# Performance work log

Hardware: AMD Instinct MI355X
Metric: run time of the kernel (lower is better)

The kernel has to match this reference:

```python
import jax, jax.numpy as jnp
import numpy as np

B, T, S, D, VOCAB = 16, 64, 128, 512, 32000


def setup_inputs():
    key = jax.random.key(0)
    ks = jax.random.split(key, 20)
    w = lambda i, shape: jax.random.normal(ks[i], shape, dtype=jnp.float32) * 0.05
    return {
        'words': jax.random.randint(ks[0], (B, T), 0, VOCAB),
        'encoder_output': jax.random.normal(ks[1], (B, S, D), dtype=jnp.float32),
        'pre_h': jax.random.normal(ks[2], (B, D), dtype=jnp.float32),
        'cell': jax.random.normal(ks[3], (B, D), dtype=jnp.float32),
        'emb': w(4, (VOCAB, D)),
        'W_ih': w(5, (4 * D, D)), 'W_hh': w(6, (4 * D, D)),
        'b_ih': w(7, (4 * D,)), 'b_hh': w(8, (4 * D,)),
        'Wh_w': w(9, (D, D)),
        'Ws_w': w(10, (D, D)), 'Ws_b': w(11, (D,)),
        'vt_w': w(12, (D,)),
        'V_w': w(13, (D, 2 * D)), 'V_b': w(14, (D,)),
        'Vp_w': w(15, (VOCAB, D)), 'Vp_b': w(16, (VOCAB,)),
    }


def lstm(xs, h0, c0, W_ih, W_hh, b_ih, b_hh):
    # xs: [T, B, D]; PyTorch LSTM gate order: i, f, g, o
    def step(carry, x_t):
        h, c = carry
        g = x_t @ W_ih.T + b_ih + h @ W_hh.T + b_hh
        i, f, gg, o = jnp.split(g, 4, axis=-1)
        c = jax.nn.sigmoid(f) * c + jax.nn.sigmoid(i) * jnp.tanh(gg)
        h = jax.nn.sigmoid(o) * jnp.tanh(c)
        return (h, c), h
    _, hs = jax.lax.scan(step, (h0, c0), xs)
    return hs


def reference(words, encoder_output, pre_h, cell, emb, W_ih, W_hh, b_ih, b_hh,
              Wh_w, Ws_w, Ws_b, vt_w, V_w, V_b, Vp_w, Vp_b):
    x = emb[words]                                   # [B, T, D]
    hs = lstm(x.transpose(1, 0, 2), pre_h, cell, W_ih, W_hh, b_ih, b_hh)
    out = hs.transpose(1, 0, 2)                      # [B, T, D] decoder states
    wh = encoder_output @ Wh_w.T                     # [B, S, D]
    ws = out @ Ws_w.T + Ws_b                         # [B, T, D]
    # Bahdanau additive attention scores e[b,s,t] = v_t . tanh(wh[b,s] + ws[b,t])
    e = jnp.einsum('bstd,d->bst', jnp.tanh(wh[:, :, None, :] + ws[:, None, :, :]), vt_w)
    a = jax.nn.softmax(e, axis=1)                    # softmax over source positions
    context = jnp.einsum('bst,bsd->btd', a, encoder_output)
    cat = jnp.concatenate([context, out], axis=-1)   # [B, T, 2D]
    return (cat @ V_w.T + V_b) @ Vp_w.T + Vp_b       # [B, T, VOCAB]
```

## Files before the change

### kernel.cpp

```cpp
#include <hip/hip_runtime.h>

#define DEV __device__ __forceinline__

typedef float f32x4 __attribute__((ext_vector_type(4)));
typedef short s16x8 __attribute__((ext_vector_type(8)));
typedef unsigned short u16;
typedef u16 u16x4 __attribute__((ext_vector_type(4)));
typedef u16 u16x8 __attribute__((ext_vector_type(8)));
typedef unsigned int u32x4 __attribute__((ext_vector_type(4)));

constexpr int Bb = 16, Tt = 64, Ss = 128, Dd = 512, Vv = 32000, FD = 2048;

DEV u16 f2bf(float x) {
  unsigned u = __builtin_bit_cast(unsigned, x);
  u = u + 0x7fffu + ((u >> 16) & 1u);
  return (u16)(u >> 16);
}
DEV float bf2f(u16 h) { unsigned u = ((unsigned)h) << 16; return __builtin_bit_cast(float, u); }
DEV float sigm(float x) { return 1.f / (1.f + __expf(-x)); }
DEV float ftanh(float x) {
  x = fminf(15.f, fmaxf(-15.f, x));
  float e = __expf(2.f * x);
  return (e - 1.f) / (e + 1.f);
}

__global__ void k_cvt3(const float* __restrict__ i0, u16* __restrict__ o0, int n0,
                       const float* __restrict__ i1, u16* __restrict__ o1, int n1,
                       const float* __restrict__ i2, u16* __restrict__ o2, int n2) {
  int total = n0 + n1 + n2;
  int i = blockIdx.x * blockDim.x + threadIdx.x;
  int st = gridDim.x * blockDim.x;
  for (; i < total; i += st) {
    const float* in; u16* out; int j;
    if (i < n0) { in = i0; out = o0; j = i; }
    else if (i < n0 + n1) { in = i1; out = o1; j = i - n0; }
    else { in = i2; out = o2; j = i - n0 - n1; }
    float4 v = reinterpret_cast<const float4*>(in)[j];
    u16x4 o;
    o.x = f2bf(v.x); o.y = f2bf(v.y); o.z = f2bf(v.z); o.w = f2bf(v.w);
    reinterpret_cast<u16x4*>(out)[j] = o;
  }
}

DEV void cvt_split_one(const float* __restrict__ in, u16* __restrict__ hi,
                       u16* __restrict__ lo, int i) {
  float4 v = reinterpret_cast<const float4*>(in)[i];
  u16x4 oh, ol;
  float vv[4] = {v.x, v.y, v.z, v.w};
#pragma unroll
  for (int j = 0; j < 4; ++j) {
    u16 h = f2bf(vv[j]);
    oh[j] = h;
    ol[j] = f2bf(vv[j] - bf2f(h));
  }
  reinterpret_cast<u16x4*>(hi)[i] = oh;
  reinterpret_cast<u16x4*>(lo)[i] = ol;
}

__global__ void k_cvt_split(const float* __restrict__ in, u16* __restrict__ hi,
                            u16* __restrict__ lo, int n4) {
  int i = blockIdx.x * blockDim.x + threadIdx.x;
  int st = gridDim.x * blockDim.x;
  for (; i < n4; i += st) cvt_split_one(in, hi, lo, i);
}

__global__ void k_cvt_split2(const float* __restrict__ a, u16* __restrict__ ah, u16* __restrict__ al,
                             const float* __restrict__ b, u16* __restrict__ bh, u16* __restrict__ bl,
                             int n4) {
  int i = blockIdx.x * blockDim.x + threadIdx.x;
  int st = gridDim.x * blockDim.x;
  if (blockIdx.y == 0) { for (; i < n4; i += st) cvt_split_one(a, ah, al, i); }
  else                 { for (; i < n4; i += st) cvt_split_one(b, bh, bl, i); }
}

__global__ void k_prep(const int* __restrict__ words, const float* __restrict__ emb,
                       u16* __restrict__ xb,
                       const float* __restrict__ pre, unsigned* __restrict__ hp0,
                       const float* __restrict__ bi, const float* __restrict__ bh,
                       float* __restrict__ bsum) {
  int blk = blockIdx.x, tid = threadIdx.x;
  if (blk < Bb * Tt) {
    int row = words[blk];
    int d = tid * 2;
    float2 v = *reinterpret_cast<const float2*>(&emb[(size_t)row * Dd + d]);
    xb[(size_t)blk * Dd + d] = f2bf(v.x);
    xb[(size_t)blk * Dd + d + 1] = f2bf(v.y);
  } else if (blk < Bb * Tt + 32) {
    int i = (blk - Bb * Tt) * 256 + tid;
    float v = pre[i];
    u16 h = f2bf(v);
    u16 l = f2bf(v - bf2f(h));
    hp0[i] = (unsigned)h | ((unsigned)l << 16);
  } else {
    int i = (blk - Bb * Tt - 32) * 256 + tid;
    bsum[i] = bi[i] + bh[i];
  }
}

template <bool BIAS, bool OUTBF, int TERMS>
__global__ __launch_bounds__(256) void k_gemm(const u16* __restrict__ A,
                                              const u16* __restrict__ Al,
                                              const u16* __restrict__ Bm,
                                              const u16* __restrict__ Bl,
                                              float* __restrict__ Cf, u16* __restrict__ Cb,
                                              const float* __restrict__ bias,
                                              int M, int N, int K) {
  constexpr int NTILE = (TERMS == 3) ? 4 : 2;
  __shared__ u16 ls[NTILE * 128 * 32];
  u16* lsA = ls;
  u16* lsB = ls + 128 * 32;
  u16* lsAl = ls + 2 * 128 * 32;
  u16* lsBl = ls + 3 * 128 * 32;
  const int mt = M >> 7;
  const int tm = (blockIdx.x % mt) << 7;
  const int tn = (blockIdx.x / mt) << 7;
  const int tid = threadIdx.x;
  const int wave = tid >> 6, lane = tid & 63;
  const int wr = wave >> 1, wc = wave & 1;
  f32x4 acc[4][4];
#pragma unroll
  for (int i = 0; i < 4; ++i)
#pragma unroll
    for (int j = 0; j < 4; ++j) acc[i][j] = (f32x4){0.f, 0.f, 0.f, 0.f};

  const int lrow = lane >> 2;
  const int lk = (lane & 3) << 3;
  const int fr = lane & 15, fk = (lane >> 4) << 3;

  for (int k0 = 0; k0 < K; k0 += 32) {
#pragma unroll
    for (int r = 0; r < 2; ++r) {
      int rowA = r * 64 + wave * 16;
      size_t goffA = (size_t)(tm + rowA + lrow) * K + k0 + lk;
      size_t goffB = (size_t)(tn + rowA + lrow) * K + k0 + lk;
      __builtin_amdgcn_global_load_lds((const __attribute__((address_space(1))) void*)(A + goffA),
                                       (__attribute__((address_space(3))) void*)&lsA[rowA * 32],
                                       16, 0, 0);
      __builtin_amdgcn_global_load_lds((const __attribute__((address_space(1))) void*)(Bm + goffB),
                                       (__attribute__((address_space(3))) void*)&lsB[rowA * 32],
                                       16, 0, 0);
      if constexpr (TERMS == 3) {
        __builtin_amdgcn_global_load_lds((const __attribute__((address_space(1))) void*)(Al + goffA),
                                         (__attribute__((address_space(3))) void*)&lsAl[rowA * 32],
                                         16, 0, 0);
        __builtin_amdgcn_global_load_lds((const __attribute__((address_space(1))) void*)(Bl + goffB),
                                         (__attribute__((address_space(3))) void*)&lsBl[rowA * 32],
                                         16, 0, 0);
      }
    }
    __syncthreads();
    s16x8 av[4], bv[4];
#pragma unroll
    for (int mi = 0; mi < 4; ++mi)
      av[mi] = *reinterpret_cast<const s16x8*>(&lsA[(wr * 64 + mi * 16 + fr) * 32 + fk]);
#pragma unroll
    for (int ni = 0; ni < 4; ++ni)
      bv[ni] = *reinterpret_cast<const s16x8*>(&lsB[(wc * 64 + ni * 16 + fr) * 32 + fk]);
    if constexpr (TERMS == 3) {
      s16x8 avl[4], bvl[4];
#pragma unroll
      for (int mi = 0; mi < 4; ++mi)
        avl[mi] = *reinterpret_cast<const s16x8*>(&lsAl[(wr * 64 + mi * 16 + fr) * 32 + fk]);
#pragma unroll
      for (int ni = 0; ni < 4; ++ni)
        bvl[ni] = *reinterpret_cast<const s16x8*>(&lsBl[(wc * 64 + ni * 16 + fr) * 32 + fk]);
#pragma unroll
      for (int mi = 0; mi < 4; ++mi)
#pragma unroll
        for (int ni = 0; ni < 4; ++ni) {
          acc[mi][ni] = __builtin_amdgcn_mfma_f32_16x16x32_bf16(av[mi], bv[ni], acc[mi][ni], 0, 0, 0);
          acc[mi][ni] = __builtin_amdgcn_mfma_f32_16x16x32_bf16(av[mi], bvl[ni], acc[mi][ni], 0, 0, 0);
          acc[mi][ni] = __builtin_amdgcn_mfma_f32_16x16x32_bf16(avl[mi], bv[ni], acc[mi][ni], 0, 0, 0);
        }
    } else {
#pragma unroll
      for (int mi = 0; mi < 4; ++mi)
#pragma unroll
        for (int ni = 0; ni < 4; ++ni)
          acc[mi][ni] = __builtin_amdgcn_mfma_f32_16x16x32_bf16(av[mi], bv[ni], acc[mi][ni], 0, 0, 0);
    }
    __syncthreads();
  }

  const int fm = (lane >> 4) << 2;
#pragma unroll
  for (int ni = 0; ni < 4; ++ni) {
    int col = tn + wc * 64 + ni * 16 + fr;
    float badd = 0.f;
    if constexpr (BIAS) badd = bias[col];
#pragma unroll
    for (int mi = 0; mi < 4; ++mi) {
#pragma unroll
      for (int r = 0; r < 4; ++r) {
        int row = tm + wr * 64 + mi * 16 + fm + r;
        size_t idx = (size_t)row * N + col;
        float v = acc[mi][ni][r] + badd;
        if constexpr (OUTBF) Cb[idx] = f2bf(v);
        else Cf[idx] = v;
      }
    }
  }
}

__global__ __launch_bounds__(256) void k_lstm(const float* __restrict__ xg,
                                              const float* __restrict__ Whh,
                                              const float* __restrict__ cell,
                                              unsigned* __restrict__ hpack,
                                              u16* __restrict__ out_hi,
                                              u16* __restrict__ out_lo,
                                              int* __restrict__ flags) {
  const int w = blockIdx.x;
  const int tid = threadIdx.x;
  const int gi = tid >> 6, lane = tid & 63;
  const int ds0 = w << 4;
  __shared__ float g_lds[4][16][16];

  const int fr = lane & 15;
  const int fkb = (lane >> 4) << 3;

  s16x8 whi[16], wlo[16];
  {
    const float* wrow = Whh + (size_t)(gi * Dd + ds0 + fr) * Dd;
#pragma unroll
    for (int kc = 0; kc < 16; ++kc) {
      int k = kc * 32 + fkb;
      float4 a = *reinterpret_cast<const float4*>(&wrow[k]);
      float4 b = *reinterpret_cast<const float4*>(&wrow[k + 4]);
      float vv[8] = {a.x, a.y, a.z, a.w, b.x, b.y, b.z, b.w};
#pragma unroll
      for (int j = 0; j < 8; ++j) {
        u16 h = f2bf(vv[j]);
        whi[kc][j] = (short)h;
        wlo[kc][j] = (short)f2bf(vv[j] - bf2f(h));
      }
    }
  }

  const int ub = tid >> 4, ud = tid & 15;
  float c = cell[(size_t)ub * Dd + ds0 + ud];

  for (int t = 0; t < Tt; ++t) {
    float xgv[4];
#pragma unroll
    for (int r = 0; r < 4; ++r) {
      int bb = ((lane >> 4) << 2) + r;
      xgv[r] = xg[(size_t)(bb * Tt + t) * FD + gi * Dd + ds0 + fr];
    }
#pragma unroll
    for (int r = 0; r < 4; ++r) asm volatile("" ::"v"(xgv[r]));

    if (t > 0) {
      if (gi == 0) {
        if (lane < 32 && lane != w) {
          while (__hip_atomic_load(&flags[lane * 32], __ATOMIC_RELAXED,
                                   __HIP_MEMORY_SCOPE_AGENT) < t) {}
          while (__hip_atomic_load(&flags[lane * 32], __ATOMIC_ACQUIRE,
                                   __HIP_MEMORY_SCOPE_AGENT) < t) {}
        }
        __builtin_amdgcn_sched_barrier(0);
      }
      __syncthreads();
    }

    const unsigned* hp = hpack + (size_t)t * (Bb * Dd) + (size_t)fr * Dd;
    f32x4 a0 = (f32x4){0.f, 0.f, 0.f, 0.f};
    f32x4 a1 = a0, a2 = a0;
#pragma unroll
    for (int kc = 0; kc < 16; ++kc) {
      int k = kc * 32 + fkb;
      u32x4 u0 = *reinterpret_cast<const u32x4*>(&hp[k]);
      u32x4 u1 = *reinterpret_cast<const u32x4*>(&hp[k + 4]);
      s16x8 ahi, alo;
#pragma unroll
      for (int j = 0; j < 4; ++j) {
        ahi[j] = (short)(u0[j] & 0xffffu); alo[j] = (short)(u0[j] >> 16);
        ahi[4 + j] = (short)(u1[j] & 0xffffu); alo[4 + j] = (short)(u1[j] >> 16);
      }
      a0 = __builtin_amdgcn_mfma_f32_16x16x32_bf16(ahi, whi[kc], a0, 0, 0, 0);
      a1 = __builtin_amdgcn_mfma_f32_16x16x32_bf16(ahi, wlo[kc], a1, 0, 0, 0);
      a2 = __builtin_amdgcn_mfma_f32_16x16x32_bf16(alo, whi[kc], a2, 0, 0, 0);
    }
#pragma unroll
    for (int r = 0; r < 4; ++r) {
      int bb = ((lane >> 4) << 2) + r;
      g_lds[gi][bb][fr] = a0[r] + a1[r] + a2[r] + xgv[r];
    }
    __syncthreads();
    float iv = g_lds[0][ub][ud], fv = g_lds[1][ub][ud];
    float gv = g_lds[2][ub][ud], ov = g_lds[3][ub][ud];
    c = sigm(fv) * c + sigm(iv) * ftanh(gv);
    float h = sigm(ov) * ftanh(c);
    u16 hh = f2bf(h);
    u16 hl = f2bf(h - bf2f(hh));
    unsigned pk = (unsigned)hh | ((unsigned)hl << 16);
    __hip_atomic_store(&hpack[(size_t)(t + 1) * (Bb * Dd) + ub * Dd + ds0 + ud], pk,
                       __ATOMIC_RELAXED, __HIP_MEMORY_SCOPE_AGENT);
    size_t oidx = (size_t)(ub * Tt + t) * Dd + ds0 + ud;
    out_hi[oidx] = hh;
    out_lo[oidx] = hl;
    __syncthreads();
    if (tid == 0)
      __hip_atomic_store(&flags[w * 32], t + 1, __ATOMIC_RELAXED, __HIP_MEMORY_SCOPE_AGENT);
  }
}

__global__ __launch_bounds__(256) void k_attn(const float* __restrict__ wh,
                                              const float* __restrict__ wst,
                                              const float* __restrict__ vt,
                                              const float* __restrict__ enc,
                                              const u16* __restrict__ out_hi,
                                              u16* __restrict__ cat) {
  const int tid = threadIdx.x;
  const int wave = tid >> 6, lane = tid & 63;
  const int wid = blockIdx.x * 4 + wave;
  const int b = wid >> 6, t = wid & 63;
  const int d0 = lane << 3;

  float wsv[8], vtv[8];
  {
    const float4* p = reinterpret_cast<const float4*>(&wst[(size_t)(b * Tt + t) * Dd + d0]);
    float4 x = p[0], y = p[1];
    wsv[0] = x.x; wsv[1] = x.y; wsv[2] = x.z; wsv[3] = x.w;
    wsv[4] = y.x; wsv[5] = y.y; wsv[6] = y.z; wsv[7] = y.w;
    const float4* q = reinterpret_cast<const float4*>(&vt[d0]);
    float4 u = q[0], v = q[1];
    vtv[0] = u.x; vtv[1] = u.y; vtv[2] = u.z; vtv[3] = u.w;
    vtv[4] = v.x; vtv[5] = v.y; vtv[6] = v.z; vtv[7] = v.w;
  }
  float e0 = 0.f, e1 = 0.f;
  for (int s = 0; s < Ss; ++s) {
    const float4* p = reinterpret_cast<const float4*>(&wh[(size_t)(b * Ss + s) * Dd + d0]);
    float4 x = p[0], y = p[1];
    float whv[8] = {x.x, x.y, x.z, x.w, y.x, y.y, y.z, y.w};
    float a = 0.f;
#pragma unroll
    for (int j = 0; j < 8; ++j) a += ftanh(whv[j] + wsv[j]) * vtv[j];
#pragma unroll
    for (int off = 32; off; off >>= 1) a += __shfl_xor(a, off);
    if (lane == (s & 63)) { if (s < 64) e0 = a; else e1 = a; }
  }
  float m = fmaxf(e0, e1);
#pragma unroll
  for (int off = 32; off; off >>= 1) m = fmaxf(m, __shfl_xor(m, off));
  float p0 = __expf(e0 - m), p1 = __expf(e1 - m);
  float sum = p0 + p1;
#pragma unroll
  for (int off = 32; off; off >>= 1) sum += __shfl_xor(sum, off);
  float inv = 1.f / sum;
  float a0 = p0 * inv, a1 = p1 * inv;

  float ctx[8] = {0.f, 0.f, 0.f, 0.f, 0.f, 0.f, 0.f, 0.f};
  for (int s = 0; s < Ss; ++s) {
    float as = __shfl(s < 64 ? a0 : a1, s & 63);
    const float4* p = reinterpret_cast<const float4*>(&enc[(size_t)(b * Ss + s) * Dd + d0]);
    float4 x = p[0], y = p[1];
    ctx[0] += as * x.x; ctx[1] += as * x.y; ctx[2] += as * x.z; ctx[3] += as * x.w;
    ctx[4] += as * y.x; ctx[5] += as * y.y; ctx[6] += as * y.z; ctx[7] += as * y.w;
  }
  u16x8 co;
#pragma unroll
  for (int j = 0; j < 8; ++j) co[j] = f2bf(ctx[j]);
  size_t cbase = (size_t)(b * Tt + t) * (2 * Dd);
  *reinterpret_cast<u16x8*>(&cat[cbase + d0]) = co;
  u16x8 ov = *reinterpret_cast<const u16x8*>(&out_hi[(size_t)(b * Tt + t) * Dd + d0]);
  *reinterpret_cast<u16x8*>(&cat[cbase + Dd + d0]) = ov;
}

extern "C" void kernel_launch(void* const* d_in, const int* in_sizes, int n_in,
                              void* d_out, int out_size, void* d_ws, size_t ws_size,
                              hipStream_t stream) {
  const int* words = (const int*)d_in[0];
  const float* enc = (const float*)d_in[1];
  const float* pre_h = (const float*)d_in[2];
  const float* cell = (const float*)d_in[3];
  const float* emb = (const float*)d_in[4];
  const float* W_ih = (const float*)d_in[5];
  const float* W_hh = (const float*)d_in[6];
  const float* b_ih = (const float*)d_in[7];
  const float* b_hh = (const float*)d_in[8];
  const float* Wh_w = (const float*)d_in[9];
  const float* Ws_w = (const float*)d_in[10];
  const float* Ws_b = (const float*)d_in[11];
  const float* vt_w = (const float*)d_in[12];
  const float* V_w = (const float*)d_in[13];
  const float* V_b = (const float*)d_in[14];
  const float* Vp_w = (const float*)d_in[15];
  const float* Vp_b = (const float*)d_in[16];
  float* outp = (float*)d_out;

  char* ws = (char*)d_ws;
  size_t off = 0;
  auto alloc = [&](size_t bytes) {
    char* p = ws + off;
    off = (off + bytes + 255) & ~(size_t)255;
    return p;
  };
  int* flags = (int*)alloc(4096);
  float* xg = (float*)alloc((size_t)Bb * Tt * FD * 4);
  float* wh = (float*)alloc((size_t)Bb * Ss * Dd * 4);
  float* wst = (float*)alloc((size_t)Bb * Tt * Dd * 4);
  unsigned* hpack = (unsigned*)alloc((size_t)(Tt + 1) * Bb * Dd * 4);
  u16* out_hi = (u16*)alloc((size_t)Bb * Tt * Dd * 2);
  u16* out_lo = (u16*)alloc((size_t)Bb * Tt * Dd * 2);
  u16* x_bf = (u16*)alloc((size_t)Bb * Tt * Dd * 2);
  u16* enc_hi = (u16*)alloc((size_t)Bb * Ss * Dd * 2);
  u16* enc_lo = (u16*)alloc((size_t)Bb * Ss * Dd * 2);
  u16* Wih_bf = (u16*)alloc((size_t)FD * Dd * 2);
  u16* Whw_hi = (u16*)alloc((size_t)Dd * Dd * 2);
  u16* Whw_lo = (u16*)alloc((size_t)Dd * Dd * 2);
  u16* Wsw_hi = (u16*)alloc((size_t)Dd * Dd * 2);
  u16* Wsw_lo = (u16*)alloc((size_t)Dd * Dd * 2);
  u16* Vw_bf = (u16*)alloc((size_t)Dd * 2 * Dd * 2);
  u16* Vp_bf = (u16*)alloc((size_t)Vv * Dd * 2);
  u16* cat = (u16*)alloc((size_t)Bb * Tt * 2 * Dd * 2);
  u16* hmid = (u16*)alloc((size_t)Bb * Tt * Dd * 2);
  float* bsum = (float*)alloc((size_t)FD * 4);
  if (off > ws_size) return;

  hipMemsetAsync(flags, 0, 4096, stream);

  k_cvt3<<<2048, 256, 0, stream>>>(W_ih, Wih_bf, FD * Dd / 4,
                                   V_w, Vw_bf, Dd * 2 * Dd / 4,
                                   Vp_w, Vp_bf, Vv * Dd / 4);
  k_cvt_split<<<1024, 256, 0, stream>>>(enc, enc_hi, enc_lo, Bb * Ss * Dd / 4);
  k_cvt_split2<<<dim3(256, 2), 256, 0, stream>>>(Wh_w, Whw_hi, Whw_lo,
                                                 Ws_w, Wsw_hi, Wsw_lo, Dd * Dd / 4);
  k_prep<<<Bb * Tt + 32 + 8, 256, 0, stream>>>(words, emb, x_bf, pre_h, (unsigned*)hpack,
                                               b_ih, b_hh, bsum);

  k_gemm<true, false, 1><<<8 * 16, 256, 0, stream>>>(x_bf, nullptr, Wih_bf, nullptr,
                                                     xg, nullptr, bsum, 1024, 2048, 512);
  k_gemm<false, false, 3><<<16 * 4, 256, 0, stream>>>(enc_hi, enc_lo, Whw_hi, Whw_lo,
                                                      wh, nullptr, nullptr, 2048, 512, 512);
  k_lstm<<<32, 256, 0, stream>>>(xg, W_hh, cell, (unsigned*)hpack, out_hi, out_lo, flags);
  k_gemm<true, false, 3><<<8 * 4, 256, 0, stream>>>(out_hi, out_lo, Wsw_hi, Wsw_lo,
                                                    wst, nullptr, Ws_b, 1024, 512, 512);
  k_attn<<<256, 256, 0, stream>>>(wh, wst, vt_w, enc, out_hi, cat);
  k_gemm<true, true, 1><<<8 * 4, 256, 0, stream>>>(cat, nullptr, Vw_bf, nullptr,
                                                   nullptr, hmid, V_b, 1024, 512, 1024);
  k_gemm<true, false, 1><<<8 * 250, 256, 0, stream>>>(hmid, nullptr, Vp_bf, nullptr,
                                                      outp, nullptr, Vp_b, 1024, 32000, 512);
}
```

Baseline: 629.9 us.

## Overlap LSTM recurrence with Wh GEMM and weight conversions in one launch

Merges the sequential LSTM kernel with the encoder Wh projection GEMM and the conversion of Vp, V and Ws weights into one 256-block launch, with blocks dispatched by index. The idle GPU capacity during the latency-bound 32-block recurrence is used for independent work that previously ran serially. The pre-LSTM conversions are also merged into a single kernel. This risks the LSTM blocks' spin-wait progress depending on co-resident blocks, and contention for memory bandwidth slowing the critical recurrence path.

```diff
diff --git a/kernel.cpp b/kernel.cpp
--- a/kernel.cpp
+++ b/kernel.cpp
@@ -24,22 +24,11 @@
   return (e - 1.f) / (e + 1.f);
 }
 
-__global__ void k_cvt3(const float* __restrict__ i0, u16* __restrict__ o0, int n0,
-                       const float* __restrict__ i1, u16* __restrict__ o1, int n1,
-                       const float* __restrict__ i2, u16* __restrict__ o2, int n2) {
-  int total = n0 + n1 + n2;
-  int i = blockIdx.x * blockDim.x + threadIdx.x;
-  int st = gridDim.x * blockDim.x;
-  for (; i < total; i += st) {
-    const float* in; u16* out; int j;
-    if (i < n0) { in = i0; out = o0; j = i; }
-    else if (i < n0 + n1) { in = i1; out = o1; j = i - n0; }
-    else { in = i2; out = o2; j = i - n0 - n1; }
-    float4 v = reinterpret_cast<const float4*>(in)[j];
-    u16x4 o;
-    o.x = f2bf(v.x); o.y = f2bf(v.y); o.z = f2bf(v.z); o.w = f2bf(v.w);
-    reinterpret_cast<u16x4*>(out)[j] = o;
-  }
+DEV void cvt_plain_one(const float* __restrict__ in, u16* __restrict__ out, int i) {
+  float4 v = reinterpret_cast<const float4*>(in)[i];
+  u16x4 o;
+  o.x = f2bf(v.x); o.y = f2bf(v.y); o.z = f2bf(v.z); o.w = f2bf(v.w);
+  reinterpret_cast<u16x4*>(out)[i] = o;
 }
 
 DEV void cvt_split_one(const float* __restrict__ in, u16* __restrict__ hi,
@@ -57,20 +46,19 @@
   reinterpret_cast<u16x4*>(lo)[i] = ol;
 }
 
-__global__ void k_cvt_split(const float* __restrict__ in, u16* __restrict__ hi,
-                            u16* __restrict__ lo, int n4) {
+__global__ void k_cvt_pre(const float* __restrict__ Wih, u16* __restrict__ Wih_bf, int n0,
+                          const float* __restrict__ enc, u16* __restrict__ ench,
+                          u16* __restrict__ encl, int n1,
+                          const float* __restrict__ Whw, u16* __restrict__ whh,
+                          u16* __restrict__ whl, int n2) {
+  int total = n0 + n1 + n2;
   int i = blockIdx.x * blockDim.x + threadIdx.x;
   int st = gridDim.x * blockDim.x;
-  for (; i < n4; i += st) cvt_split_one(in, hi, lo, i);
-}
-
-__global__ void k_cvt_split2(const float* __restrict__ a, u16* __restrict__ ah, u16* __restrict__ al,
-                             const float* __restrict__ b, u16* __restrict__ bh, u16* __restrict__ bl,
-                             int n4) {
-  int i = blockIdx.x * blockDim.x + threadIdx.x;
-  int st = gridDim.x * blockDim.x;
-  if (blockIdx.y == 0) { for (; i < n4; i += st) cvt_split_one(a, ah, al, i); }
-  else                 { for (; i < n4; i += st) cvt_split_one(b, bh, bl, i); }
+  for (; i < total; i += st) {
+    if (i < n0) cvt_plain_one(Wih, Wih_bf, i);
+    else if (i < n0 + n1) cvt_split_one(enc, ench, encl, i - n0);
+    else cvt_split_one(Whw, whh, whl, i - n0 - n1);
+  }
 }
 
 __global__ void k_prep(const int* __restrict__ words, const float* __restrict__ emb,
@@ -98,23 +86,18 @@
 }
 
 template <bool BIAS, bool OUTBF, int TERMS>
-__global__ __launch_bounds__(256) void k_gemm(const u16* __restrict__ A,
-                                              const u16* __restrict__ Al,
-                                              const u16* __restrict__ Bm,
-                                              const u16* __restrict__ Bl,
-                                              float* __restrict__ Cf, u16* __restrict__ Cb,
-                                              const float* __restrict__ bias,
-                                              int M, int N, int K) {
-  constexpr int NTILE = (TERMS == 3) ? 4 : 2;
-  __shared__ u16 ls[NTILE * 128 * 32];
+DEV void gemm_body(u16* ls, int tile, int tid,
+                   const u16* __restrict__ A, const u16* __restrict__ Al,
+                   const u16* __restrict__ Bm, const u16* __restrict__ Bl,
+                   float* __restrict__ Cf, u16* __restrict__ Cb,
+                   const float* __restrict__ bias, int M, int N, int K) {
   u16* lsA = ls;
   u16* lsB = ls + 128 * 32;
   u16* lsAl = ls + 2 * 128 * 32;
   u16* lsBl = ls + 3 * 128 * 32;
   const int mt = M >> 7;
-  const int tm = (blockIdx.x % mt) << 7;
-  const int tn = (blockIdx.x / mt) << 7;
-  const int tid = threadIdx.x;
+  const int tm = (tile % mt) << 7;
+  const int tn = (tile / mt) << 7;
   const int wave = tid >> 6, lane = tid & 63;
   const int wr = wave >> 1, wc = wave & 1;
   f32x4 acc[4][4];
@@ -202,18 +185,26 @@
   }
 }
 
-__global__ __launch_bounds__(256) void k_lstm(const float* __restrict__ xg,
-                                              const float* __restrict__ Whh,
-                                              const float* __restrict__ cell,
-                                              unsigned* __restrict__ hpack,
-                                              u16* __restrict__ out_hi,
-                                              u16* __restrict__ out_lo,
-                                              int* __restrict__ flags) {
-  const int w = blockIdx.x;
-  const int tid = threadIdx.x;
+template <bool BIAS, bool OUTBF, int TERMS>
+__global__ __launch_bounds__(256) void k_gemm(const u16* __restrict__ A,
+                                              const u16* __restrict__ Al,
+                                              const u16* __restrict__ Bm,
+                                              const u16* __restrict__ Bl,
+                                              float* __restrict__ Cf, u16* __restrict__ Cb,
+                                              const float* __restrict__ bias,
+                                              int M, int N, int K) {
+  __shared__ u16 ls[4 * 128 * 32];
+  gemm_body<BIAS, OUTBF, TERMS>(ls, blockIdx.x, threadIdx.x, A, Al, Bm, Bl, Cf, Cb, bias, M, N, K);
+}
+
+DEV void lstm_body(int w, int tid, float* gls,
+                   const float* __restrict__ xg, const float* __restrict__ Whh,
+                   const float* __restrict__ cell, unsigned* __restrict__ hpack,
+                   u16* __restrict__ out_hi, u16* __restrict__ out_lo,
+                   int* __restrict__ flags) {
   const int gi = tid >> 6, lane = tid & 63;
   const int ds0 = w << 4;
-  __shared__ float g_lds[4][16][16];
+  float (*g_lds)[16][16] = (float(*)[16][16])gls;
 
   const int fr = lane & 15;
   const int fkb = (lane >> 4) << 3;
@@ -301,6 +292,36 @@
     __syncthreads();
     if (tid == 0)
       __hip_atomic_store(&flags[w * 32], t + 1, __ATOMIC_RELAXED, __HIP_MEMORY_SCOPE_AGENT);
+  }
+}
+
+__global__ __launch_bounds__(256) void k_lstm_fused(
+    const float* __restrict__ xg, const float* __restrict__ Whh,
+    const float* __restrict__ cell, unsigned* __restrict__ hpack,
+    u16* __restrict__ out_hi, u16* __restrict__ out_lo, int* __restrict__ flags,
+    const u16* __restrict__ enc_hi, const u16* __restrict__ enc_lo,
+    const u16* __restrict__ Whw_hi, const u16* __restrict__ Whw_lo,
+    float* __restrict__ wh,
+    const float* __restrict__ Vp_w, u16* __restrict__ Vp_bf,
+    const float* __restrict__ V_w, u16* __restrict__ Vw_bf,
+    const float* __restrict__ Ws_w, u16* __restrict__ Wsw_hi, u16* __restrict__ Wsw_lo) {
+  __shared__ u16 ls[4 * 128 * 32];
+  const int blk = blockIdx.x, tid = threadIdx.x;
+  if (blk < 32) {
+    lstm_body(blk, tid, (float*)ls, xg, Whh, cell, hpack, out_hi, out_lo, flags);
+  } else if (blk < 96) {
+    gemm_body<false, false, 3>(ls, blk - 32, tid, enc_hi, enc_lo, Whw_hi, Whw_lo,
+                               wh, nullptr, nullptr, 2048, 512, 512);
+  } else {
+    const int nVp = Vv * Dd / 4, nV = Dd * 2 * Dd / 4, nWs = Dd * Dd / 4;
+    int total = nVp + nV + nWs;
+    int i = (blk - 96) * 256 + tid;
+    int st = 160 * 256;
+    for (; i < total; i += st) {
+      if (i < nVp) cvt_plain_one(Vp_w, Vp_bf, i);
+      else if (i < nVp + nV) cvt_plain_one(V_w, Vw_bf, i - nVp);
+      else cvt_split_one(Ws_w, Wsw_hi, Wsw_lo, i - nVp - nV);
+    }
   }
 }
 
@@ -419,20 +440,16 @@
 
   hipMemsetAsync(flags, 0, 4096, stream);
 
-  k_cvt3<<<2048, 256, 0, stream>>>(W_ih, Wih_bf, FD * Dd / 4,
-                                   V_w, Vw_bf, Dd * 2 * Dd / 4,
-                                   Vp_w, Vp_bf, Vv * Dd / 4);
-  k_cvt_split<<<1024, 256, 0, stream>>>(enc, enc_hi, enc_lo, Bb * Ss * Dd / 4);
-  k_cvt_split2<<<dim3(256, 2), 256, 0, stream>>>(Wh_w, Whw_hi, Whw_lo,
-                                                 Ws_w, Wsw_hi, Wsw_lo, Dd * Dd / 4);
+  k_cvt_pre<<<256, 256, 0, stream>>>(W_ih, Wih_bf, FD * Dd / 4,
+                                     enc, enc_hi, enc_lo, Bb * Ss * Dd / 4,
+                                     Wh_w, Whw_hi, Whw_lo, Dd * Dd / 4);
   k_prep<<<Bb * Tt + 32 + 8, 256, 0, stream>>>(words, emb, x_bf, pre_h, (unsigned*)hpack,
                                                b_ih, b_hh, bsum);
-
   k_gemm<true, false, 1><<<8 * 16, 256, 0, stream>>>(x_bf, nullptr, Wih_bf, nullptr,
                                                      xg, nullptr, bsum, 1024, 2048, 512);
-  k_gemm<false, false, 3><<<16 * 4, 256, 0, stream>>>(enc_hi, enc_lo, Whw_hi, Whw_lo,
-                                                      wh, nullptr, nullptr, 2048, 512, 512);
-  k_lstm<<<32, 256, 0, stream>>>(xg, W_hh, cell, (unsigned*)hpack, out_hi, out_lo, flags);
+  k_lstm_fused<<<256, 256, 0, stream>>>(xg, W_hh, cell, (unsigned*)hpack, out_hi, out_lo,
+                                        flags, enc_hi, enc_lo, Whw_hi, Whw_lo, wh,
+                                        Vp_w, Vp_bf, V_w, Vw_bf, Ws_w, Wsw_hi, Wsw_lo);
   k_gemm<true, false, 3><<<8 * 4, 256, 0, stream>>>(out_hi, out_lo, Wsw_hi, Wsw_lo,
                                                     wst, nullptr, Ws_b, 1024, 512, 512);
   k_attn<<<256, 256, 0, stream>>>(wh, wst, vt_w, enc, out_hi, cat);
```

New measurement: 592.0 us. 1.06x faster.
